# Kernel optimization log

Hardware: AMD Instinct MI355X
Metric: run time of the kernel (lower is better)

The kernel has to match this reference:

```python
import jax, jax.numpy as jnp
import numpy as np

B, S, E = 2, 2048, 2048
NQ, NKV, HD = 16, 4, 128
WINDOW = 512
ROPE_BASE = 10000.0


def _rope(x):
    # x: [B, H, S, HD], interleaved even/odd rotation
    half = HD // 2
    freqs = 1.0 / (ROPE_BASE ** (2.0 * jnp.arange(half, dtype=jnp.float32) / HD))
    pos = jnp.arange(x.shape[2], dtype=jnp.float32)
    ang = pos[:, None] * freqs[None, :]            # [S, HD/2]
    cos = jnp.cos(ang)[None, None].astype(x.dtype)  # [1,1,S,HD/2]
    sin = jnp.sin(ang)[None, None].astype(x.dtype)
    xe = x[..., 0::2]
    xo = x[..., 1::2]
    re = xe * cos - xo * sin
    ro = xe * sin + xo * cos
    return jnp.stack([re, ro], axis=-1).reshape(x.shape)


def setup_inputs() -> dict:
    key = jax.random.key(0)
    ks = jax.random.split(key, 9)
    s_in = 1.0 / np.sqrt(E)
    s_out = 1.0 / np.sqrt(NQ * HD)
    return {
        "x": jax.random.normal(ks[0], (B, S, E), jnp.float32),
        "Wq": jax.random.normal(ks[1], (E, NQ * HD), jnp.float32) * s_in,
        "bq": jax.random.normal(ks[2], (NQ * HD,), jnp.float32) * 0.01,
        "Wk": jax.random.normal(ks[3], (E, NKV * HD), jnp.float32) * s_in,
        "bk": jax.random.normal(ks[4], (NKV * HD,), jnp.float32) * 0.01,
        "Wv": jax.random.normal(ks[5], (E, NKV * HD), jnp.float32) * s_in,
        "bv": jax.random.normal(ks[6], (NKV * HD,), jnp.float32) * 0.01,
        "Wo": jax.random.normal(ks[7], (NQ * HD, E), jnp.float32) * s_out,
        "bo": jax.random.normal(ks[8], (E,), jnp.float32) * 0.01,
    }


def reference(x, Wq, bq, Wk, bk, Wv, bv, Wo, bo):
    b, s, _ = x.shape
    q = (x @ Wq + bq).reshape(b, s, NQ, HD).transpose(0, 2, 1, 3)   # [B,NQ,S,HD]
    k = (x @ Wk + bk).reshape(b, s, NKV, HD).transpose(0, 2, 1, 3)  # [B,NKV,S,HD]
    v = (x @ Wv + bv).reshape(b, s, NKV, HD).transpose(0, 2, 1, 3)
    q = _rope(q)
    k = _rope(k)
    rep = NQ // NKV
    k = jnp.repeat(k, rep, axis=1)  # [B,NQ,S,HD], matches torch repeat pattern
    v = jnp.repeat(v, rep, axis=1)
    scores = jnp.einsum("bhqd,bhkd->bhqk", q, k) / np.sqrt(HD)
    i = jnp.arange(s)[:, None]
    j = jnp.arange(s)[None, :]
    allowed = (j <= i) & ((i - j) <= WINDOW)  # sliding-window causal mask
    scores = jnp.where(allowed[None, None], scores, -jnp.inf)
    weights = jax.nn.softmax(scores, axis=-1)
    out = jnp.einsum("bhqk,bhkd->bhqd", weights, v)
    out = out.transpose(0, 2, 1, 3).reshape(b, s, NQ * HD)
    return out @ Wo + bo
```

## Files before the change

kernel.cpp:

```cpp
#include <hip/hip_runtime.h>
#include <hip/hip_bf16.h>
#include <math.h>

#define BB 2
#define SS 2048
#define EE 2048
#define NQ 16
#define NKV 4
#define HD 128
#define WINDOW 512

typedef __hip_bfloat16 bf16;
typedef short short8 __attribute__((ext_vector_type(8)));
typedef float f32x4 __attribute__((ext_vector_type(4)));

__device__ __forceinline__ float toF(bf16 v) { return __bfloat162float(v); }
__device__ __forceinline__ bf16 toB(float v) { return __float2bfloat16(v); }

__device__ __forceinline__ void gld_lds16(const void* g, void* l) {
    __builtin_amdgcn_global_load_lds(
        (const __attribute__((address_space(1))) void*)g,
        (__attribute__((address_space(3))) void*)l, 16, 0, 0);
}

__global__ __launch_bounds__(256) void convert_bf16(const float* __restrict__ in,
                                                    bf16* __restrict__ out, int n) {
    int i = (blockIdx.x * 256 + threadIdx.x) * 4;
    if (i >= n) return;
    const float4 v = *(const float4*)(in + i);
    bf16 o[4] = {toB(v.x), toB(v.y), toB(v.z), toB(v.w)};
    *(uint2*)(out + i) = *(const uint2*)o;
}

__global__ __launch_bounds__(256) void convert_transpose(const float* __restrict__ in,
                                                         bf16* __restrict__ out,
                                                         int K, int N) {
    __shared__ float tile[32][33];
    const int t = threadIdx.x;
    const int tx = t & 31, ty = t >> 5;
    const int n0 = blockIdx.x * 32, k0 = blockIdx.y * 32;
#pragma unroll
    for (int r = 0; r < 4; r++)
        tile[ty + r * 8][tx] = in[(size_t)(k0 + ty + r * 8) * N + n0 + tx];
    __syncthreads();
#pragma unroll
    for (int r = 0; r < 4; r++)
        out[(size_t)(n0 + ty + r * 8) * K + k0 + tx] = toB(tile[tx][ty + r * 8]);
}

__global__ __launch_bounds__(256) void convert_transpose_qkv(
    const float* __restrict__ Wq, const float* __restrict__ Wk,
    const float* __restrict__ Wv, bf16* __restrict__ out) {
    __shared__ float tile[32][33];
    const int t = threadIdx.x;
    const int tx = t & 31, ty = t >> 5;
    const int n0 = blockIdx.x * 32, k0 = blockIdx.y * 32;
    const float* src; int N, nl0;
    if (n0 < 2048)      { src = Wq; N = 2048; nl0 = n0; }
    else if (n0 < 2560) { src = Wk; N = 512;  nl0 = n0 - 2048; }
    else                { src = Wv; N = 512;  nl0 = n0 - 2560; }
#pragma unroll
    for (int r = 0; r < 4; r++)
        tile[ty + r * 8][tx] = src[(size_t)(k0 + ty + r * 8) * N + nl0 + tx];
    __syncthreads();
#pragma unroll
    for (int r = 0; r < 4; r++)
        out[(size_t)(n0 + ty + r * 8) * 2048 + k0 + tx] = toB(tile[tx][ty + r * 8]);
}

template <int MODE>
__global__ __launch_bounds__(256) void mfma_gemm(
    const bf16* __restrict__ A, const bf16* __restrict__ BT,
    const float* __restrict__ b0, const float* __restrict__ b1,
    const float* __restrict__ b2,
    float* __restrict__ Yf,
    bf16* __restrict__ Yq, bf16* __restrict__ Yk, bf16* __restrict__ Yv,
    int M, int N, int K) {
    __shared__ bf16 As[128 * 32];
    __shared__ bf16 Bs[128 * 32];

    const int t = threadIdx.x;
    const int lane = t & 63;
    const int w = t >> 6;
    const int wm = w >> 1, wn = w & 1;
    const int m0 = blockIdx.y * 128, n0 = blockIdx.x * 128;

    const int srow = lane >> 2;
    const int sg   = lane & 3;
    const int scol = (sg ^ ((srow >> 1) & 3)) * 8;

    f32x4 acc[4][4];
#pragma unroll
    for (int i = 0; i < 4; i++)
#pragma unroll
        for (int j = 0; j < 4; j++) acc[i][j] = (f32x4)0.f;

    const int lr = lane & 15;
    const int lq = lane >> 4;
    const int slotr = (lq ^ ((lr >> 1) & 3)) * 8;

    for (int k0 = 0; k0 < K; k0 += 32) {
#pragma unroll
        for (int s = 0; s < 2; s++) {
            const int c = w * 2 + s;
            gld_lds16(A + (size_t)(m0 + c * 16 + srow) * K + k0 + scol, As + c * 512);
            gld_lds16(BT + (size_t)(n0 + c * 16 + srow) * K + k0 + scol, Bs + c * 512);
        }
        __syncthreads();
        short8 af[4], bfv[4];
#pragma unroll
        for (int i = 0; i < 4; i++)
            af[i] = *(const short8*)(As + (wm * 64 + i * 16 + lr) * 32 + slotr);
#pragma unroll
        for (int j = 0; j < 4; j++)
            bfv[j] = *(const short8*)(Bs + (wn * 64 + j * 16 + lr) * 32 + slotr);
#pragma unroll
        for (int i = 0; i < 4; i++)
#pragma unroll
            for (int j = 0; j < 4; j++)
                acc[i][j] = __builtin_amdgcn_mfma_f32_16x16x32_bf16(af[i], bfv[j],
                                                                    acc[i][j], 0, 0, 0);
        __syncthreads();
    }

    if (MODE == 0) {
#pragma unroll
        for (int j = 0; j < 4; j++) {
            const int col = n0 + wn * 64 + j * 16 + lr;
            const float bj = b0[col];
#pragma unroll
            for (int i = 0; i < 4; i++) {
                const int row = m0 + wm * 64 + i * 16 + lq * 4;
#pragma unroll
                for (int r = 0; r < 4; r++)
                    Yf[(size_t)(row + r) * N + col] = acc[i][j][r] + bj;
            }
        }
    } else {
        bf16* outp; const float* bias; int ldc, c0; bool dorope;
        if (n0 < 2048)      { outp = Yq; bias = b0; ldc = 2048; c0 = n0;        dorope = true; }
        else if (n0 < 2560) { outp = Yk; bias = b1; ldc = 512;  c0 = n0 - 2048; dorope = true; }
        else                { outp = Yv; bias = b2; ldc = 512;  c0 = n0 - 2560; dorope = false; }
#pragma unroll
        for (int j = 0; j < 4; j++) {
            const int col = c0 + wn * 64 + j * 16 + lr;
            const float bj = bias[col];
            if (dorope) {
                const int d2 = (col & 127) >> 1;
                const bool odd = col & 1;
                const float freq = __expf(-0.14384103622589045f * (float)d2);
#pragma unroll
                for (int i = 0; i < 4; i++) {
                    const int row = m0 + wm * 64 + i * 16 + lq * 4;
#pragma unroll
                    for (int r = 0; r < 4; r++) {
                        const float v = acc[i][j][r] + bj;
                        const float p = __shfl_xor(v, 1, 64);
                        const float ang = (float)((row + r) & (SS - 1)) * freq;
                        float sn, cs;
                        __sincosf(ang, &sn, &cs);
                        const float o = odd ? (p * sn + v * cs) : (v * cs - p * sn);
                        outp[(size_t)(row + r) * ldc + col] = toB(o);
                    }
                }
            } else {
#pragma unroll
                for (int i = 0; i < 4; i++) {
                    const int row = m0 + wm * 64 + i * 16 + lq * 4;
#pragma unroll
                    for (int r = 0; r < 4; r++)
                        outp[(size_t)(row + r) * ldc + col] = toB(acc[i][j][r] + bj);
                }
            }
        }
    }
}

__global__ __launch_bounds__(256) void attn_mfma(const bf16* __restrict__ Q,
                                                 const bf16* __restrict__ K,
                                                 const bf16* __restrict__ V,
                                                 bf16* __restrict__ Oout) {
    __shared__ bf16 Ks[64 * 128];
    __shared__ bf16 Vt[128 * 72];
    __shared__ bf16 Ps[4 * 16 * 72];

    const int t = threadIdx.x;
    const int lane = t & 63;
    const int w = t >> 6;
    const int q0 = blockIdx.x * 64;
    const int h = blockIdx.y;
    const int b = blockIdx.z;
    const int hkv = h >> 2;
    const int lr = lane & 15;
    const int lq = lane >> 4;
    const float scale = 0.08838834764831845f;

    short8 aq[4];
    {
        const int q = q0 + w * 16 + lr;
        const bf16* qp = Q + (((size_t)b * SS + q) * NQ + h) * HD + lq * 8;
#pragma unroll
        for (int ks = 0; ks < 4; ks++) aq[ks] = *(const short8*)(qp + ks * 32);
    }

    f32x4 Oa[8];
#pragma unroll
    for (int nb = 0; nb < 8; nb++) Oa[nb] = (f32x4)0.f;
    float mprev[4] = {-3.0e38f, -3.0e38f, -3.0e38f, -3.0e38f};
    float lsum[4] = {0.f, 0.f, 0.f, 0.f};

    bf16* Pw = Ps + w * 16 * 72;
    const int jstart = (q0 >= WINDOW) ? (q0 - WINDOW) : 0;

    for (int c0 = jstart; c0 <= q0; c0 += 64) {
        __syncthreads();
#pragma unroll
        for (int s = 0; s < 4; s++) {
            const bf16* gk = K +
                (((size_t)b * SS + c0 + w * 16 + s * 4 + (lane >> 4)) * NKV + hkv) * HD +
                (lane & 15) * 8;
            gld_lds16(gk, Ks + (w * 16 + s * 4) * 128);
        }
        {
            const int key = t & 63;
            const int dg = (t >> 6) * 8;
            const bf16* gv = V + (((size_t)b * SS + c0 + key) * NKV + hkv) * HD + dg;
#pragma unroll
            for (int it = 0; it < 4; it++) {
                short8 vv = *(const short8*)(gv + it * 32);
#pragma unroll
                for (int j = 0; j < 8; j++)
                    Vt[(dg + it * 32 + j) * 72 + key] = ((const bf16*)&vv)[j];
            }
        }
        __syncthreads();

        f32x4 sa[4];
#pragma unroll
        for (int nb = 0; nb < 4; nb++) sa[nb] = (f32x4)0.f;
#pragma unroll
        for (int ks = 0; ks < 4; ks++) {
#pragma unroll
            for (int nb = 0; nb < 4; nb++) {
                short8 bk = *(const short8*)(Ks + (nb * 16 + lr) * 128 + ks * 32 + lq * 8);
                sa[nb] = __builtin_amdgcn_mfma_f32_16x16x32_bf16(aq[ks], bk, sa[nb], 0, 0, 0);
            }
        }

        const int rowb = q0 + w * 16 + lq * 4;
        float pr[4][4], alpha[4];
#pragma unroll
        for (int r = 0; r < 4; r++) {
            const int row = rowb + r;
            float sv[4];
            float mx = -3.0e38f;
#pragma unroll
            for (int nb = 0; nb < 4; nb++) {
                const int col = c0 + nb * 16 + lr;
                const bool valid = (col <= row) && (row - col <= WINDOW);
                const float s = valid ? sa[nb][r] * scale : -3.0e38f;
                sv[nb] = s;
                mx = fmaxf(mx, s);
            }
#pragma unroll
            for (int off = 1; off < 16; off <<= 1) mx = fmaxf(mx, __shfl_xor(mx, off, 64));
            const float mn = fmaxf(fmaxf(mprev[r], mx), -1.0e30f);
            alpha[r] = __expf(mprev[r] - mn);
            mprev[r] = mn;
            float rs = 0.f;
#pragma unroll
            for (int nb = 0; nb < 4; nb++) {
                const float p = __expf(sv[nb] - mn);
                pr[r][nb] = p;
                rs += p;
            }
#pragma unroll
            for (int off = 1; off < 16; off <<= 1) rs += __shfl_xor(rs, off, 64);
            lsum[r] = lsum[r] * alpha[r] + rs;
        }

#pragma unroll
        for (int r = 0; r < 4; r++)
#pragma unroll
            for (int nb = 0; nb < 4; nb++)
                Pw[(lq * 4 + r) * 72 + nb * 16 + lr] = toB(pr[r][nb]);

#pragma unroll
        for (int nb = 0; nb < 8; nb++)
#pragma unroll
            for (int r = 0; r < 4; r++) Oa[nb][r] *= alpha[r];
#pragma unroll
        for (int ks = 0; ks < 2; ks++) {
            short8 pa = *(const short8*)(Pw + lr * 72 + ks * 32 + lq * 8);
#pragma unroll
            for (int nb = 0; nb < 8; nb++) {
                short8 bv = *(const short8*)(Vt + (nb * 16 + lr) * 72 + ks * 32 + lq * 8);
                Oa[nb] = __builtin_amdgcn_mfma_f32_16x16x32_bf16(pa, bv, Oa[nb], 0, 0, 0);
            }
        }
    }

    float linv[4];
#pragma unroll
    for (int r = 0; r < 4; r++) linv[r] = 1.f / lsum[r];
    const int rowb = q0 + w * 16 + lq * 4;
#pragma unroll
    for (int nb = 0; nb < 8; nb++)
#pragma unroll
        for (int r = 0; r < 4; r++)
            Oout[(((size_t)b * SS + rowb + r) * NQ + h) * HD + nb * 16 + lr] =
                toB(Oa[nb][r] * linv[r]);
}

extern "C" void kernel_launch(void* const* d_in, const int* in_sizes, int n_in,
                              void* d_out, int out_size, void* d_ws, size_t ws_size,
                              hipStream_t stream) {
    const float* x  = (const float*)d_in[0];
    const float* Wq = (const float*)d_in[1];
    const float* bq = (const float*)d_in[2];
    const float* Wk = (const float*)d_in[3];
    const float* bk = (const float*)d_in[4];
    const float* Wv = (const float*)d_in[5];
    const float* bv = (const float*)d_in[6];
    const float* Wo = (const float*)d_in[7];
    const float* bo = (const float*)d_in[8];
    float* out = (float*)d_out;

    const int M   = BB * SS;
    const int DQ  = NQ * HD;
    const int DKV = NKV * HD;
    const int NPK = DQ + 2 * DKV;

    bf16* xb     = (bf16*)d_ws;
    bf16* WqkvT  = xb + (size_t)M * EE;
    bf16* WoT    = WqkvT + (size_t)NPK * EE;
    bf16* Qb     = WoT + (size_t)EE * DQ;
    bf16* Kb     = Qb + (size_t)M * DQ;
    bf16* Vb     = Kb + (size_t)M * DKV;

    convert_bf16<<<(M * EE / 4 + 255) / 256, 256, 0, stream>>>(x, xb, M * EE);
    convert_transpose_qkv<<<dim3(NPK / 32, EE / 32), 256, 0, stream>>>(Wq, Wk, Wv, WqkvT);
    convert_transpose<<<dim3(DQ / 32, DQ / 32), 256, 0, stream>>>(Wo, WoT, DQ, EE);

    mfma_gemm<1><<<dim3(NPK / 128, M / 128), 256, 0, stream>>>(
        xb, WqkvT, bq, bk, bv, nullptr, Qb, Kb, Vb, M, NPK, EE);

    attn_mfma<<<dim3(SS / 64, NQ, BB), 256, 0, stream>>>(Qb, Kb, Vb, Qb);

    mfma_gemm<0><<<dim3(EE / 128, M / 128), 256, 0, stream>>>(
        Qb, WoT, bo, nullptr, nullptr, out, nullptr, nullptr, nullptr, M, EE, DQ);
}
```

Measured before the change: 333.1 us.

## Store V transposed from projection and async-load swizzled K/V tiles into LDS

The QKV projection epilogue now writes V in a [B,NKV,HD,S] transposed layout with packed 4-element stores. The attention kernel can then load V (and K) straight into LDS through global_load_lds, using an XOR swizzle instead of a per-element transposing scatter through registers. It also skips the mask arithmetic for fully-unmasked tiles. The aim is to cut LDS bank conflicts and the costly V transpose in the inner loop. The trade-off is strided, less coalesced V writes in the projection epilogue.

```diff
diff --git a/kernel.cpp b/kernel.cpp
--- a/kernel.cpp
+++ b/kernel.cpp
@@ -136,41 +136,47 @@
                     Yf[(size_t)(row + r) * N + col] = acc[i][j][r] + bj;
             }
         }
-    } else {
-        bf16* outp; const float* bias; int ldc, c0; bool dorope;
-        if (n0 < 2048)      { outp = Yq; bias = b0; ldc = 2048; c0 = n0;        dorope = true; }
-        else if (n0 < 2560) { outp = Yk; bias = b1; ldc = 512;  c0 = n0 - 2048; dorope = true; }
-        else                { outp = Yv; bias = b2; ldc = 512;  c0 = n0 - 2560; dorope = false; }
+    } else if (n0 < 2560) {
+        bf16* outp; const float* bias; int ldc, c0;
+        if (n0 < 2048) { outp = Yq; bias = b0; ldc = 2048; c0 = n0; }
+        else           { outp = Yk; bias = b1; ldc = 512;  c0 = n0 - 2048; }
 #pragma unroll
         for (int j = 0; j < 4; j++) {
             const int col = c0 + wn * 64 + j * 16 + lr;
             const float bj = bias[col];
-            if (dorope) {
-                const int d2 = (col & 127) >> 1;
-                const bool odd = col & 1;
-                const float freq = __expf(-0.14384103622589045f * (float)d2);
-#pragma unroll
-                for (int i = 0; i < 4; i++) {
-                    const int row = m0 + wm * 64 + i * 16 + lq * 4;
-#pragma unroll
-                    for (int r = 0; r < 4; r++) {
-                        const float v = acc[i][j][r] + bj;
-                        const float p = __shfl_xor(v, 1, 64);
-                        const float ang = (float)((row + r) & (SS - 1)) * freq;
-                        float sn, cs;
-                        __sincosf(ang, &sn, &cs);
-                        const float o = odd ? (p * sn + v * cs) : (v * cs - p * sn);
-                        outp[(size_t)(row + r) * ldc + col] = toB(o);
-                    }
+            const int d2 = (col & 127) >> 1;
+            const bool odd = col & 1;
+            const float freq = __expf(-0.14384103622589045f * (float)d2);
+#pragma unroll
+            for (int i = 0; i < 4; i++) {
+                const int row = m0 + wm * 64 + i * 16 + lq * 4;
+#pragma unroll
+                for (int r = 0; r < 4; r++) {
+                    const float v = acc[i][j][r] + bj;
+                    const float p = __shfl_xor(v, 1, 64);
+                    const float ang = (float)((row + r) & (SS - 1)) * freq;
+                    float sn, cs;
+                    __sincosf(ang, &sn, &cs);
+                    const float o = odd ? (p * sn + v * cs) : (v * cs - p * sn);
+                    outp[(size_t)(row + r) * ldc + col] = toB(o);
                 }
-            } else {
-#pragma unroll
-                for (int i = 0; i < 4; i++) {
-                    const int row = m0 + wm * 64 + i * 16 + lq * 4;
-#pragma unroll
-                    for (int r = 0; r < 4; r++)
-                        outp[(size_t)(row + r) * ldc + col] = toB(acc[i][j][r] + bj);
-                }
+            }
+        }
+    } else {
+        const int c0 = n0 - 2560;
+#pragma unroll
+        for (int j = 0; j < 4; j++) {
+            const int col = c0 + wn * 64 + j * 16 + lr;
+            const float bj = b2[col];
+            const int hkv = col >> 7, d = col & 127;
+#pragma unroll
+            for (int i = 0; i < 4; i++) {
+                const int row = m0 + wm * 64 + i * 16 + lq * 4;
+                const int bb = row >> 11, sr = row & (SS - 1);
+                union { bf16 b[4]; uint2 u; } o4;
+#pragma unroll
+                for (int r = 0; r < 4; r++) o4.b[r] = toB(acc[i][j][r] + bj);
+                *(uint2*)(Yv + (((size_t)bb * NKV + hkv) * HD + d) * SS + sr) = o4.u;
             }
         }
     }
@@ -178,10 +184,10 @@
 
 __global__ __launch_bounds__(256) void attn_mfma(const bf16* __restrict__ Q,
                                                  const bf16* __restrict__ K,
-                                                 const bf16* __restrict__ V,
+                                                 const bf16* __restrict__ VT,
                                                  bf16* __restrict__ Oout) {
     __shared__ bf16 Ks[64 * 128];
-    __shared__ bf16 Vt[128 * 72];
+    __shared__ bf16 Vs[128 * 64];
     __shared__ bf16 Ps[4 * 16 * 72];
 
     const int t = threadIdx.x;
@@ -203,6 +209,11 @@
         for (int ks = 0; ks < 4; ks++) aq[ks] = *(const short8*)(qp + ks * 32);
     }
 
+    const int krow = w * 16 + (lane >> 4);
+    const int vrow = w * 32 + (lane >> 3);
+    const bf16* Kbase = K + ((size_t)b * SS * NKV + hkv) * HD;
+    const bf16* Vbase = VT + (((size_t)b * NKV + hkv) * HD) * SS;
+
     f32x4 Oa[8];
 #pragma unroll
     for (int nb = 0; nb < 8; nb++) Oa[nb] = (f32x4)0.f;
@@ -216,22 +227,17 @@
         __syncthreads();
 #pragma unroll
         for (int s = 0; s < 4; s++) {
-            const bf16* gk = K +
-                (((size_t)b * SS + c0 + w * 16 + s * 4 + (lane >> 4)) * NKV + hkv) * HD +
-                (lane & 15) * 8;
-            gld_lds16(gk, Ks + (w * 16 + s * 4) * 128);
-        }
-        {
-            const int key = t & 63;
-            const int dg = (t >> 6) * 8;
-            const bf16* gv = V + (((size_t)b * SS + c0 + key) * NKV + hkv) * HD + dg;
-#pragma unroll
-            for (int it = 0; it < 4; it++) {
-                short8 vv = *(const short8*)(gv + it * 32);
-#pragma unroll
-                for (int j = 0; j < 8; j++)
-                    Vt[(dg + it * 32 + j) * 72 + key] = ((const bf16*)&vv)[j];
-            }
+            const int r_ = krow + s * 4;
+            const int g_ = (lane & 15) ^ (r_ & 7);
+            gld_lds16(Kbase + (size_t)(c0 + r_) * (NKV * HD) + g_ * 8,
+                      Ks + (w * 16 + s * 4) * 128);
+        }
+#pragma unroll
+        for (int s = 0; s < 4; s++) {
+            const int d_ = vrow + s * 8;
+            const int g_ = (lane & 7) ^ (d_ & 7);
+            gld_lds16(Vbase + (size_t)d_ * SS + c0 + g_ * 8,
+                      Vs + (w * 32 + s * 8) * 64);
         }
         __syncthreads();
 
@@ -242,25 +248,37 @@
         for (int ks = 0; ks < 4; ks++) {
 #pragma unroll
             for (int nb = 0; nb < 4; nb++) {
-                short8 bk = *(const short8*)(Ks + (nb * 16 + lr) * 128 + ks * 32 + lq * 8);
+                const int slot = (ks * 4 + lq) ^ (lr & 7);
+                short8 bk = *(const short8*)(Ks + (nb * 16 + lr) * 128 + slot * 8);
                 sa[nb] = __builtin_amdgcn_mfma_f32_16x16x32_bf16(aq[ks], bk, sa[nb], 0, 0, 0);
             }
         }
 
         const int rowb = q0 + w * 16 + lq * 4;
+        const bool noMask = (c0 + 63 <= q0 + w * 16) &&
+                            (q0 + w * 16 + 15 - c0 <= WINDOW);
         float pr[4][4], alpha[4];
 #pragma unroll
         for (int r = 0; r < 4; r++) {
             const int row = rowb + r;
             float sv[4];
             float mx = -3.0e38f;
-#pragma unroll
-            for (int nb = 0; nb < 4; nb++) {
-                const int col = c0 + nb * 16 + lr;
-                const bool valid = (col <= row) && (row - col <= WINDOW);
-                const float s = valid ? sa[nb][r] * scale : -3.0e38f;
-                sv[nb] = s;
-                mx = fmaxf(mx, s);
+            if (noMask) {
+#pragma unroll
+                for (int nb = 0; nb < 4; nb++) {
+                    const float s = sa[nb][r] * scale;
+                    sv[nb] = s;
+                    mx = fmaxf(mx, s);
+                }
+            } else {
+#pragma unroll
+                for (int nb = 0; nb < 4; nb++) {
+                    const int col = c0 + nb * 16 + lr;
+                    const bool valid = (col <= row) && (row - col <= WINDOW);
+                    const float s = valid ? sa[nb][r] * scale : -3.0e38f;
+                    sv[nb] = s;
+                    mx = fmaxf(mx, s);
+                }
             }
 #pragma unroll
             for (int off = 1; off < 16; off <<= 1) mx = fmaxf(mx, __shfl_xor(mx, off, 64));
@@ -294,7 +312,8 @@
             short8 pa = *(const short8*)(Pw + lr * 72 + ks * 32 + lq * 8);
 #pragma unroll
             for (int nb = 0; nb < 8; nb++) {
-                short8 bv = *(const short8*)(Vt + (nb * 16 + lr) * 72 + ks * 32 + lq * 8);
+                const int slot = (ks * 4 + lq) ^ (lr & 7);
+                short8 bv = *(const short8*)(Vs + (nb * 16 + lr) * 64 + slot * 8);
                 Oa[nb] = __builtin_amdgcn_mfma_f32_16x16x32_bf16(pa, bv, Oa[nb], 0, 0, 0);
             }
         }
```

After: 333.0 us. About the same (-0.0%).
